# Optimization experiments

Measured on AMD Instinct MI355X. Metric: run time of the kernel, lower is better.

## Reference

```python
import jax, jax.numpy as jnp
import numpy as np


def setup_inputs() -> dict:
    key = jax.random.key(0)
    k1, k2, k3, k4, k5 = jax.random.split(key, 5)
    B, C, H, W = 8, 256, 64, 64
    Cp = C // 8  # query/key channels
    x = jax.random.normal(k1, (B, C, H, W), dtype=jnp.float32)
    # 1x1 conv weights (bias=False in the module), spectral norm treated as a fixed weight scale
    Wq = jax.random.normal(k2, (Cp, C), dtype=jnp.float32) * 0.05
    Wk = jax.random.normal(k3, (Cp, C), dtype=jnp.float32) * 0.05
    Wv = jax.random.normal(k4, (C, C), dtype=jnp.float32) * 0.05
    gamma = jax.random.normal(k5, (1,), dtype=jnp.float32)
    return {"x": x, "Wq": Wq, "Wk": Wk, "Wv": Wv, "gamma": gamma}


def reference(x, Wq, Wk, Wv, gamma):
    B, C, H, W = x.shape
    xf = x.reshape(B, C, H * W)  # (B, C, N)
    # ConvLayer = 1x1 conv (no bias) followed by ReLU
    f = jax.nn.relu(jnp.einsum('oc,bcn->bon', Wq, xf))  # (B, C', N)
    g = jax.nn.relu(jnp.einsum('oc,bcn->bon', Wk, xf))  # (B, C', N)
    h = jax.nn.relu(jnp.einsum('oc,bcn->bon', Wv, xf))  # (B, C, N)
    # beta = softmax(f^T g, dim=1): normalize over the FIRST N axis (faithful to source)
    scores = jnp.einsum('bcn,bcm->bnm', f, g)  # (B, N, N)
    beta = jax.nn.softmax(scores, axis=1)
    o = gamma * jnp.einsum('bcn,bnm->bcm', h, beta) + xf  # (B, C, N)
    return o.reshape(B, C, H, W)
```

## Files before the change

kernel.cpp:

```cpp
#include <hip/hip_runtime.h>


typedef __attribute__((ext_vector_type(8))) short bf16x8;
typedef __attribute__((ext_vector_type(4))) float f32x4;
typedef __attribute__((ext_vector_type(4))) unsigned short us4;

#define LOG2E 1.44269504088896f

static __device__ __forceinline__ unsigned short f2bf(float x) {
    union { float f; unsigned u; } v; v.f = x;
    unsigned r = v.u + 0x7FFFu + ((v.u >> 16) & 1u);
    return (unsigned short)(r >> 16);
}
static __device__ __forceinline__ float bf2f(unsigned short u) {
    union { unsigned u; float f; } v; v.u = ((unsigned)u) << 16;
    return v.f;
}

__global__ __launch_bounds__(256) void wconv_kernel(
    const float* __restrict__ Wq, const float* __restrict__ Wk,
    const float* __restrict__ Wv, unsigned short* __restrict__ wq,
    unsigned short* __restrict__ wk, unsigned short* __restrict__ wv)
{
    const int i = blockIdx.x * 256 + threadIdx.x;
    if (i < 8192)            wq[i] = f2bf(Wq[i] * LOG2E);
    else if (i < 16384)      wk[i - 8192] = f2bf(Wk[i - 8192]);
    else                     wv[i - 16384] = f2bf(Wv[i - 16384]);
}

#define XPITCH 264
__global__ __launch_bounds__(256, 2) void producer_kernel(
    const float* __restrict__ x, const unsigned short* __restrict__ wq,
    const unsigned short* __restrict__ wk, const unsigned short* __restrict__ wv,
    unsigned short* __restrict__ f_t, unsigned short* __restrict__ g_t,
    unsigned short* __restrict__ h_bf, float* __restrict__ normg,
    unsigned* __restrict__ maxnf_u)
{
    __shared__ unsigned short x_s[64 * XPITCH];
    __shared__ unsigned short fg_s[4 * 2 * 512];

    const int tid  = threadIdx.x;
    const int w    = tid >> 6;
    const int lane = tid & 63;
    const int q    = lane >> 4;
    const int r    = lane & 15;
    const int b    = blockIdx.y;
    const int n0   = blockIdx.x << 6;
    const size_t bN = (size_t)b << 12;
    const f32x4 zero = {0.f, 0.f, 0.f, 0.f};

#pragma unroll
    for (int jj = 0; jj < 4; jj++) {
        const int task = jj * 256 + tid;
        const int n4 = task & 15;
        const int c4 = task >> 4;
        float va[4][4];
#pragma unroll
        for (int i = 0; i < 4; i++) {
            const float4 v = ((const float4*)(x + ((size_t)b << 20)
                              + (size_t)(c4 * 4 + i) * 4096 + n0))[n4];
            va[i][0] = v.x; va[i][1] = v.y; va[i][2] = v.z; va[i][3] = v.w;
        }
#pragma unroll
        for (int i = 0; i < 4; i++) {
            us4 t;
            t.x = f2bf(va[0][i]); t.y = f2bf(va[1][i]);
            t.z = f2bf(va[2][i]); t.w = f2bf(va[3][i]);
            *(us4*)(x_s + (n4 * 4 + i) * XPITCH + c4 * 4) = t;
        }
    }
    __syncthreads();

    f32x4 acch[4][4];
    f32x4 accf[2], accg[2];
#pragma unroll
    for (int cs = 0; cs < 4; cs++)
#pragma unroll
        for (int ns = 0; ns < 4; ns++) acch[cs][ns] = zero;
    accf[0] = accf[1] = accg[0] = accg[1] = zero;

    for (int ks = 0; ks < 8; ks++) {
        const int kof = ks * 32 + q * 8;
        bf16x8 av[4], aq[2], ak[2];
#pragma unroll
        for (int cs = 0; cs < 4; cs++)
            av[cs] = *(const bf16x8*)(wv + (size_t)(w * 64 + cs * 16 + r) * 256 + kof);
#pragma unroll
        for (int ms = 0; ms < 2; ms++) {
            aq[ms] = *(const bf16x8*)(wq + (size_t)(ms * 16 + r) * 256 + kof);
            ak[ms] = *(const bf16x8*)(wk + (size_t)(ms * 16 + r) * 256 + kof);
        }
#pragma unroll
        for (int ns = 0; ns < 4; ns++) {
            const bf16x8 bx = *(const bf16x8*)(x_s + (ns * 16 + r) * XPITCH + kof);
#pragma unroll
            for (int cs = 0; cs < 4; cs++)
                acch[cs][ns] = __builtin_amdgcn_mfma_f32_16x16x32_bf16(av[cs], bx, acch[cs][ns], 0, 0, 0);
            if (ns == w) {
#pragma unroll
                for (int ms = 0; ms < 2; ms++) {
                    accf[ms] = __builtin_amdgcn_mfma_f32_16x16x32_bf16(aq[ms], bx, accf[ms], 0, 0, 0);
                    accg[ms] = __builtin_amdgcn_mfma_f32_16x16x32_bf16(ak[ms], bx, accg[ms], 0, 0, 0);
                }
            }
        }
    }

#pragma unroll
    for (int cs = 0; cs < 4; cs++)
#pragma unroll
        for (int ns = 0; ns < 4; ns++)
#pragma unroll
            for (int reg = 0; reg < 4; reg++)
                h_bf[(((size_t)b * 256 + w * 64 + cs * 16 + q * 4 + reg) << 12)
                     + n0 + ns * 16 + r] = f2bf(fmaxf(acch[cs][ns][reg], 0.f));

    unsigned short* lf = fg_s + w * 1024;
    unsigned short* lg = lf + 512;
#pragma unroll
    for (int ms = 0; ms < 2; ms++)
#pragma unroll
        for (int reg = 0; reg < 4; reg++) {
            lf[r * 32 + ms * 16 + q * 4 + reg] = f2bf(fmaxf(accf[ms][reg], 0.f));
            lg[r * 32 + ms * 16 + q * 4 + reg] = f2bf(fmaxf(accg[ms][reg], 0.f));
        }
    const bf16x8 ffrag = *(const bf16x8*)(lf + r * 32 + q * 8);
    const bf16x8 gfrag = *(const bf16x8*)(lg + r * 32 + q * 8);
    *(bf16x8*)(f_t + ((bN + n0 + w * 16 + r) << 5) + q * 8) = ffrag;
    *(bf16x8*)(g_t + ((bN + n0 + w * 16 + r) << 5) + q * 8) = gfrag;

    float nf2 = 0.f, ng2 = 0.f;
#pragma unroll
    for (int i = 0; i < 8; i++) {
        const float fv = bf2f(((unsigned short*)&ffrag)[i]);
        const float gv = bf2f(((unsigned short*)&gfrag)[i]);
        nf2 += fv * fv; ng2 += gv * gv;
    }
    nf2 += __shfl_xor(nf2, 16); nf2 += __shfl_xor(nf2, 32);
    ng2 += __shfl_xor(ng2, 16); ng2 += __shfl_xor(ng2, 32);
    if (q == 0) normg[bN + n0 + w * 16 + r] = sqrtf(ng2);
    float nf = sqrtf(nf2);
#pragma unroll
    for (int off = 1; off < 16; off <<= 1) nf = fmaxf(nf, __shfl_xor(nf, off));
    if (lane == 0) atomicMax(maxnf_u + b, __float_as_uint(nf));
}

__global__ __launch_bounds__(256, 2) void attn_kernel(
    const unsigned short* __restrict__ f_t, const unsigned short* __restrict__ g_t,
    const unsigned short* __restrict__ h_bf, const float* __restrict__ x,
    const float* __restrict__ gamma, const float* __restrict__ normg,
    const unsigned* __restrict__ maxnf_u, float* __restrict__ out)
{
    __shared__ unsigned short p_s[2][64 * 72];
    __shared__ float red_l[4][64];
    __shared__ float sLi[64];

    const int tid  = threadIdx.x;
    const int w    = tid >> 6;
    const int lane = tid & 63;
    const int q    = lane >> 4;
    const int r    = lane & 15;
    const int b    = blockIdx.y;
    const int m0   = blockIdx.x << 6;

    const size_t bN = (size_t)b << 12;
    const size_t hbase = (size_t)b << 20;
    const int c0 = w << 6;
    const f32x4 zero = {0.f, 0.f, 0.f, 0.f};

    bf16x8 bg[4];
    float Mh[4];
    const float mnf = __uint_as_float(maxnf_u[b]);
#pragma unroll
    for (int ms = 0; ms < 4; ms++) {
        bg[ms] = *(const bf16x8*)(g_t + ((bN + m0 + ms * 16 + r) << 5) + (q << 3));
        Mh[ms] = mnf * normg[bN + m0 + ms * 16 + r] * 1.0002f;
    }

    f32x4 acc[4][4];
#pragma unroll
    for (int cs = 0; cs < 4; cs++)
#pragma unroll
        for (int ms = 0; ms < 4; ms++) acc[cs][ms] = zero;
    float lt[4] = {0.f, 0.f, 0.f, 0.f};

    bf16x8 af = *(const bf16x8*)(f_t + ((bN + (w << 4) + r) << 5) + (q << 3));

    for (int t = 0; t < 64; t++) {
        const int n0 = t << 6;
        unsigned short* pb = p_s[t & 1];
        bf16x8 ah[8];
#pragma unroll
        for (int cs = 0; cs < 4; cs++) {
            const unsigned short* hp =
                h_bf + hbase + ((size_t)(c0 + cs * 16 + r) << 12) + n0 + (q << 3);
            ah[cs * 2]     = *(const bf16x8*)(hp);
            ah[cs * 2 + 1] = *(const bf16x8*)(hp + 32);
        }
        f32x4 sv[4];
#pragma unroll
        for (int ms = 0; ms < 4; ms++)
            sv[ms] = __builtin_amdgcn_mfma_f32_16x16x32_bf16(af, bg[ms], zero, 0, 0, 0);
        if (t < 63)
            af = *(const bf16x8*)(f_t + ((bN + ((t + 1) << 6) + (w << 4) + r) << 5) + (q << 3));
#pragma unroll
        for (int ms = 0; ms < 4; ms++) {
            const float e0 = __builtin_amdgcn_exp2f(sv[ms][0] - Mh[ms]);
            const float e1 = __builtin_amdgcn_exp2f(sv[ms][1] - Mh[ms]);
            const float e2 = __builtin_amdgcn_exp2f(sv[ms][2] - Mh[ms]);
            const float e3 = __builtin_amdgcn_exp2f(sv[ms][3] - Mh[ms]);
            lt[ms] += (e0 + e1) + (e2 + e3);
            uint2 pk;
            pk.x = __builtin_amdgcn_perm(__float_as_uint(e1), __float_as_uint(e0), 0x07060302u);
            pk.y = __builtin_amdgcn_perm(__float_as_uint(e3), __float_as_uint(e2), 0x07060302u);
            *(uint2*)(pb + (ms * 16 + r) * 72 + (w << 4) + (q << 2)) = pk;
        }
        __syncthreads();
#pragma unroll
        for (int ch = 0; ch < 2; ch++) {
            bf16x8 bp[4];
#pragma unroll
            for (int ms = 0; ms < 4; ms++)
                bp[ms] = *(const bf16x8*)(pb + (ms * 16 + r) * 72 + (ch << 5) + (q << 3));
#pragma unroll
            for (int cs = 0; cs < 4; cs++)
#pragma unroll
                for (int ms = 0; ms < 4; ms++)
                    acc[cs][ms] = __builtin_amdgcn_mfma_f32_16x16x32_bf16(
                        ah[cs * 2 + ch], bp[ms], acc[cs][ms], 0, 0, 0);
        }
    }

#pragma unroll
    for (int ms = 0; ms < 4; ms++) {
        lt[ms] += __shfl_xor(lt[ms], 16);
        lt[ms] += __shfl_xor(lt[ms], 32);
    }
    __syncthreads();
    if (q == 0)
#pragma unroll
        for (int ms = 0; ms < 4; ms++) red_l[w][ms * 16 + r] = lt[ms];
    __syncthreads();
    if (tid < 64)
        sLi[tid] = 1.f / (red_l[0][tid] + red_l[1][tid] + red_l[2][tid] + red_l[3][tid]);
    __syncthreads();

    const float gm = gamma[0];
#pragma unroll
    for (int cs = 0; cs < 4; cs++) {
#pragma unroll
        for (int ms = 0; ms < 4; ms++) {
            const float gl = gm * sLi[ms * 16 + r];
#pragma unroll
            for (int reg = 0; reg < 4; reg++) {
                const int c = c0 + cs * 16 + q * 4 + reg;
                const size_t a = (((size_t)b * 256 + c) << 12) + m0 + ms * 16 + r;
                out[a] = gl * acc[cs][ms][reg] + x[a];
            }
        }
    }
}

extern "C" void kernel_launch(void* const* d_in, const int* in_sizes, int n_in,
                              void* d_out, int out_size, void* d_ws, size_t ws_size,
                              hipStream_t stream) {
    const float* x     = (const float*)d_in[0];
    const float* Wq    = (const float*)d_in[1];
    const float* Wk    = (const float*)d_in[2];
    const float* Wv    = (const float*)d_in[3];
    const float* gamma = (const float*)d_in[4];
    float* out = (float*)d_out;

    char* ws = (char*)d_ws;
    unsigned short* f_t  = (unsigned short*)ws;
    unsigned short* g_t  = (unsigned short*)(ws + (2u << 20));
    unsigned short* h_bf = (unsigned short*)(ws + (4u << 20));
    float*          ng   = (float*)(ws + (20u << 20));
    unsigned*       mnf  = (unsigned*)(ws + (20u << 20) + (1u << 17));
    unsigned short* wq   = (unsigned short*)(ws + (21u << 20));
    unsigned short* wk   = wq + 8192;
    unsigned short* wv   = wk + 8192;

    hipMemsetAsync(mnf, 0, 8 * sizeof(unsigned), stream);
    wconv_kernel<<<dim3(320), 256, 0, stream>>>(Wq, Wk, Wv, wq, wk, wv);
    producer_kernel<<<dim3(64, 8), 256, 0, stream>>>(x, wq, wk, wv, f_t, g_t, h_bf, ng, mnf);
    attn_kernel<<<dim3(64, 8), 256, 0, stream>>>(f_t, g_t, h_bf, x, gamma, ng, mnf, out);
}
```

Measured before the change: 256.1 us.

## Tile h layout, software-pipeline score/exp stage with triple-buffered swizzled LDS

The producer now stages the ReLU'd h tile in shared memory and writes it out as contiguous 64x256 blocks per n-tile, replacing the scattered strided global stores. The attention kernel reads these contiguous h tiles and restructures the loop so that the scores and exp for tile t+1 are computed while the PV MFMAs consume tile t. This uses a triple-buffered, XOR-swizzled P buffer and needs only one barrier per iteration. The max subtraction is folded into the MFMA accumulator init. The goal is to overlap the softmax VALU work with the matrix work and to cut LDS bank conflicts, at the cost of extra registers and LDS.

```diff
diff --git a/kernel.cpp b/kernel.cpp
--- a/kernel.cpp
+++ b/kernel.cpp
@@ -29,6 +29,7 @@
 }
 
 #define XPITCH 264
+#define HPITCH 72
 __global__ __launch_bounds__(256, 2) void producer_kernel(
     const float* __restrict__ x, const unsigned short* __restrict__ wq,
     const unsigned short* __restrict__ wk, const unsigned short* __restrict__ wv,
@@ -36,7 +37,7 @@
     unsigned short* __restrict__ h_bf, float* __restrict__ normg,
     unsigned* __restrict__ maxnf_u)
 {
-    __shared__ unsigned short x_s[64 * XPITCH];
+    __shared__ unsigned short xh_s[256 * HPITCH];
     __shared__ unsigned short fg_s[4 * 2 * 512];
 
     const int tid  = threadIdx.x;
@@ -45,7 +46,8 @@
     const int q    = lane >> 4;
     const int r    = lane & 15;
     const int b    = blockIdx.y;
-    const int n0   = blockIdx.x << 6;
+    const int nt   = blockIdx.x;
+    const int n0   = nt << 6;
     const size_t bN = (size_t)b << 12;
     const f32x4 zero = {0.f, 0.f, 0.f, 0.f};
 
@@ -66,7 +68,7 @@
             us4 t;
             t.x = f2bf(va[0][i]); t.y = f2bf(va[1][i]);
             t.z = f2bf(va[2][i]); t.w = f2bf(va[3][i]);
-            *(us4*)(x_s + (n4 * 4 + i) * XPITCH + c4 * 4) = t;
+            *(us4*)(xh_s + (n4 * 4 + i) * XPITCH + c4 * 4) = t;
         }
     }
     __syncthreads();
@@ -92,7 +94,7 @@
         }
 #pragma unroll
         for (int ns = 0; ns < 4; ns++) {
-            const bf16x8 bx = *(const bf16x8*)(x_s + (ns * 16 + r) * XPITCH + kof);
+            const bf16x8 bx = *(const bf16x8*)(xh_s + (ns * 16 + r) * XPITCH + kof);
 #pragma unroll
             for (int cs = 0; cs < 4; cs++)
                 acch[cs][ns] = __builtin_amdgcn_mfma_f32_16x16x32_bf16(av[cs], bx, acch[cs][ns], 0, 0, 0);
@@ -106,15 +108,6 @@
         }
     }
 
-#pragma unroll
-    for (int cs = 0; cs < 4; cs++)
-#pragma unroll
-        for (int ns = 0; ns < 4; ns++)
-#pragma unroll
-            for (int reg = 0; reg < 4; reg++)
-                h_bf[(((size_t)b * 256 + w * 64 + cs * 16 + q * 4 + reg) << 12)
-                     + n0 + ns * 16 + r] = f2bf(fmaxf(acch[cs][ns][reg], 0.f));
-
     unsigned short* lf = fg_s + w * 1024;
     unsigned short* lg = lf + 512;
 #pragma unroll
@@ -143,6 +136,25 @@
 #pragma unroll
     for (int off = 1; off < 16; off <<= 1) nf = fmaxf(nf, __shfl_xor(nf, off));
     if (lane == 0) atomicMax(maxnf_u + b, __float_as_uint(nf));
+
+    __syncthreads();
+#pragma unroll
+    for (int cs = 0; cs < 4; cs++)
+#pragma unroll
+        for (int ns = 0; ns < 4; ns++)
+#pragma unroll
+            for (int reg = 0; reg < 4; reg++)
+                xh_s[(w * 64 + cs * 16 + q * 4 + reg) * HPITCH + ns * 16 + r] =
+                    f2bf(fmaxf(acch[cs][ns][reg], 0.f));
+    __syncthreads();
+    const size_t hdst = ((size_t)(b * 64 + nt)) << 14;
+#pragma unroll
+    for (int p = 0; p < 8; p++) {
+        const int c = p * 32 + (tid >> 3);
+        const int k = tid & 7;
+        *(bf16x8*)(h_bf + hdst + c * 64 + k * 8) =
+            *(const bf16x8*)(xh_s + c * HPITCH + k * 8);
+    }
 }
 
 __global__ __launch_bounds__(256, 2) void attn_kernel(
@@ -151,7 +163,7 @@
     const float* __restrict__ gamma, const float* __restrict__ normg,
     const unsigned* __restrict__ maxnf_u, float* __restrict__ out)
 {
-    __shared__ unsigned short p_s[2][64 * 72];
+    __shared__ unsigned short p_s[3][64 * 64];
     __shared__ float red_l[4][64];
     __shared__ float sLi[64];
 
@@ -164,17 +176,16 @@
     const int m0   = blockIdx.x << 6;
 
     const size_t bN = (size_t)b << 12;
-    const size_t hbase = (size_t)b << 20;
     const int c0 = w << 6;
     const f32x4 zero = {0.f, 0.f, 0.f, 0.f};
 
     bf16x8 bg[4];
-    float Mh[4];
+    float nMh[4];
     const float mnf = __uint_as_float(maxnf_u[b]);
 #pragma unroll
     for (int ms = 0; ms < 4; ms++) {
         bg[ms] = *(const bf16x8*)(g_t + ((bN + m0 + ms * 16 + r) << 5) + (q << 3));
-        Mh[ms] = mnf * normg[bN + m0 + ms * 16 + r] * 1.0002f;
+        nMh[ms] = -(mnf * normg[bN + m0 + ms * 16 + r] * 1.0002f);
     }
 
     f32x4 acc[4][4];
@@ -184,51 +195,68 @@
         for (int ms = 0; ms < 4; ms++) acc[cs][ms] = zero;
     float lt[4] = {0.f, 0.f, 0.f, 0.f};
 
-    bf16x8 af = *(const bf16x8*)(f_t + ((bN + (w << 4) + r) << 5) + (q << 3));
-
-    for (int t = 0; t < 64; t++) {
-        const int n0 = t << 6;
-        unsigned short* pb = p_s[t & 1];
-        bf16x8 ah[8];
-#pragma unroll
-        for (int cs = 0; cs < 4; cs++) {
-            const unsigned short* hp =
-                h_bf + hbase + ((size_t)(c0 + cs * 16 + r) << 12) + n0 + (q << 3);
-            ah[cs * 2]     = *(const bf16x8*)(hp);
-            ah[cs * 2 + 1] = *(const bf16x8*)(hp + 32);
-        }
-        f32x4 sv[4];
-#pragma unroll
-        for (int ms = 0; ms < 4; ms++)
-            sv[ms] = __builtin_amdgcn_mfma_f32_16x16x32_bf16(af, bg[ms], zero, 0, 0, 0);
-        if (t < 63)
-            af = *(const bf16x8*)(f_t + ((bN + ((t + 1) << 6) + (w << 4) + r) << 5) + (q << 3));
+    const int wkey = r & 7;
+    const int wchunkoff = (((((w << 1) + (q >> 1)) ^ wkey) << 3)) + ((q & 1) << 2);
+    const int rkoff0 = ((q ^ wkey) << 3);
+    const int rkoff1 = (((4 + q) ^ wkey) << 3);
+
+    auto ldf = [&](int t) {
+        return *(const bf16x8*)(f_t + ((bN + (t << 6) + (w << 4) + r) << 5) + (q << 3));
+    };
+    auto produce = [&](const bf16x8 af, unsigned short* pb) {
 #pragma unroll
         for (int ms = 0; ms < 4; ms++) {
-            const float e0 = __builtin_amdgcn_exp2f(sv[ms][0] - Mh[ms]);
-            const float e1 = __builtin_amdgcn_exp2f(sv[ms][1] - Mh[ms]);
-            const float e2 = __builtin_amdgcn_exp2f(sv[ms][2] - Mh[ms]);
-            const float e3 = __builtin_amdgcn_exp2f(sv[ms][3] - Mh[ms]);
+            f32x4 ci; ci[0] = ci[1] = ci[2] = ci[3] = nMh[ms];
+            const f32x4 sv = __builtin_amdgcn_mfma_f32_16x16x32_bf16(af, bg[ms], ci, 0, 0, 0);
+            const float e0 = __builtin_amdgcn_exp2f(sv[0]);
+            const float e1 = __builtin_amdgcn_exp2f(sv[1]);
+            const float e2 = __builtin_amdgcn_exp2f(sv[2]);
+            const float e3 = __builtin_amdgcn_exp2f(sv[3]);
             lt[ms] += (e0 + e1) + (e2 + e3);
             uint2 pk;
             pk.x = __builtin_amdgcn_perm(__float_as_uint(e1), __float_as_uint(e0), 0x07060302u);
             pk.y = __builtin_amdgcn_perm(__float_as_uint(e3), __float_as_uint(e2), 0x07060302u);
-            *(uint2*)(pb + (ms * 16 + r) * 72 + (w << 4) + (q << 2)) = pk;
-        }
+            *(uint2*)(pb + ((ms * 16 + r) << 6) + wchunkoff) = pk;
+        }
+    };
+
+    bf16x8 afn = ldf(0);
+    produce(afn, p_s[0]);
+    afn = ldf(1);
+
+    int sr = 0, sw = 1;
+    for (int t = 0; t < 64; t++) {
         __syncthreads();
-#pragma unroll
-        for (int ch = 0; ch < 2; ch++) {
-            bf16x8 bp[4];
-#pragma unroll
-            for (int ms = 0; ms < 4; ms++)
-                bp[ms] = *(const bf16x8*)(pb + (ms * 16 + r) * 72 + (ch << 5) + (q << 3));
+        const unsigned short* hb = h_bf + (((size_t)(b * 64 + t)) << 14);
+        bf16x8 ah[8];
+#pragma unroll
+        for (int cs = 0; cs < 4; cs++) {
+            const unsigned short* hp = hb + ((c0 + cs * 16 + r) << 6) + (q << 3);
+            ah[cs * 2]     = *(const bf16x8*)(hp);
+            ah[cs * 2 + 1] = *(const bf16x8*)(hp + 32);
+        }
+        if (t < 63) {
+            const bf16x8 afc = afn;
+            if (t < 62) afn = ldf(t + 2);
+            produce(afc, p_s[sw]);
+        }
+        const unsigned short* pb = p_s[sr];
+        bf16x8 bp[4][2];
+#pragma unroll
+        for (int ms = 0; ms < 4; ms++) {
+            bp[ms][0] = *(const bf16x8*)(pb + ((ms * 16 + r) << 6) + rkoff0);
+            bp[ms][1] = *(const bf16x8*)(pb + ((ms * 16 + r) << 6) + rkoff1);
+        }
+#pragma unroll
+        for (int ch = 0; ch < 2; ch++)
 #pragma unroll
             for (int cs = 0; cs < 4; cs++)
 #pragma unroll
                 for (int ms = 0; ms < 4; ms++)
                     acc[cs][ms] = __builtin_amdgcn_mfma_f32_16x16x32_bf16(
-                        ah[cs * 2 + ch], bp[ms], acc[cs][ms], 0, 0, 0);
-        }
+                        ah[cs * 2 + ch], bp[ms][ch], acc[cs][ms], 0, 0, 0);
+        sr = sw;
+        sw = (sw == 2) ? 0 : sw + 1;
     }
 
 #pragma unroll
```

After: 262.9 us. 2.6% more time.
